# Kernel optimization log

Measured on AMD Instinct MI355X. Metric: run time of the kernel, lower is better.

The kernel has to match this reference:

```python
import jax, jax.numpy as jnp
import numpy as np

FEAT_IN = 64     # len(nonterminals)
EMB = 256        # embedding_dim
K = 30           # sortk
B = 48           # batch items
NG = 11          # graphs per item (1 goal + 10 env)
G = B * NG       # 528 graphs
NPG = 192        # nodes per graph
EPG = 384        # edges per graph
N = G * NPG
E = G * EPG
D = 3 * EMB + 1  # 769, concat channel dim = conv5 kernel/stride
DENSE = (K // 2 - 5 + 1) * EMB  # 11*256 = 2816


def setup_inputs() -> dict:
    key = jax.random.key(0)
    ks = jax.random.split(key, 12)
    x = jax.random.normal(ks[0], (N, FEAT_IN), jnp.float32)
    # edges within each graph, no self loops (remove_self_loops in original)
    src_l = jax.random.randint(ks[1], (E,), 0, NPG)
    off = jax.random.randint(ks[2], (E,), 1, NPG)
    dst_l = (src_l + off) % NPG
    goff = (jnp.arange(E) // EPG) * NPG
    src = (src_l + goff).astype(jnp.int32)
    dst = (dst_l + goff).astype(jnp.int32)

    def lin(k, fi, fo):
        return (jax.random.normal(k, (fi, fo), jnp.float32) / np.float32(np.sqrt(fi)))

    return dict(
        x=x, src=src, dst=dst,
        W1=lin(ks[3], FEAT_IN, EMB), b1=jnp.zeros((EMB,), jnp.float32),
        W2=lin(ks[4], EMB, EMB), b2=jnp.zeros((EMB,), jnp.float32),
        W3=lin(ks[5], EMB, EMB), b3=jnp.zeros((EMB,), jnp.float32),
        W4=lin(ks[6], EMB, 1), b4=jnp.zeros((1,), jnp.float32),
        w5=jax.random.normal(ks[7], (EMB // 2, 1, D), jnp.float32) / np.float32(np.sqrt(D)),
        bc5=jnp.zeros((EMB // 2,), jnp.float32),
        w6=jax.random.normal(ks[8], (EMB, EMB // 2, 5), jnp.float32) / np.float32(np.sqrt(5 * EMB // 2)),
        bc6=jnp.zeros((EMB,), jnp.float32),
        Wc1=lin(ks[9], NG * DENSE, EMB), bc1=jnp.zeros((EMB,), jnp.float32),
        Wc2=lin(ks[10], EMB, 10), bc2=jnp.zeros((10,), jnp.float32),
    )


def _gcn(x, W, b, src, dst):
    # PyG GCNConv: add self loops, symmetric norm D^-1/2 (A+I) D^-1/2 (XW) + b
    h = x @ W
    deg = jnp.ones((N,), h.dtype).at[dst].add(1.0)  # +1 for self loop
    dis = jax.lax.rsqrt(deg)
    msg = h[src] * (dis[src] * dis[dst])[:, None]
    agg = jnp.zeros_like(h).at[dst].add(msg)
    return agg + h * (dis * dis)[:, None] + b  # self-loop norm = 1/deg


def _conv1d(x, w, b, stride):
    y = jax.lax.conv_general_dilated(x, w, (stride,), 'VALID',
                                     dimension_numbers=('NCH', 'OIH', 'NCH'))
    return y + b[None, :, None]


def reference(x, src, dst, W1, b1, W2, b2, W3, b3, W4, b4,
              w5, bc5, w6, bc6, Wc1, bc1, Wc2, bc2):
    x1 = jnp.tanh(_gcn(x, W1, b1, src, dst))
    x2 = jnp.tanh(_gcn(x1, W2, b2, src, dst))
    x3 = jnp.tanh(_gcn(x2, W3, b3, src, dst))
    x4 = jnp.tanh(_gcn(x3, W4, b4, src, dst))
    xc = jnp.concatenate([x1, x2, x3, x4], axis=-1)  # [N, D]
    xg = xc.reshape(G, NPG, D)
    # global_sort_pool: sort nodes per graph by last channel (desc), take top K
    _, idx = jax.lax.top_k(xg[:, :, -1], K)          # [G, K]
    xs = jnp.take_along_axis(xg, idx[:, :, None], axis=1)  # [G, K, D]
    seq = xs.reshape(G, 1, K * D)
    y = jax.nn.relu(_conv1d(seq, w5, bc5, D))        # [G, EMB/2, K]
    y = y.reshape(G, EMB // 2, K // 2, 2).max(axis=-1)  # MaxPool1d(2,2)
    y = jax.nn.relu(_conv1d(y, w6, bc6, 1))          # [G, EMB, K//2-4]
    emb = y.reshape(B, NG * DENSE)                   # 11 graphs per item, flattened
    h = jax.nn.relu(emb @ Wc1 + bc1)
    logits = h @ Wc2 + bc2                           # dropout is identity at eval
    return logits
```

## Files before the change

kernel.cpp:

```cpp
#include <hip/hip_runtime.h>
#include <hip/hip_bf16.h>

#define EMB   256
#define KSORT 30
#define BATCH 48
#define NGPI  11
#define GG    528
#define NPG   192
#define EPG   384
#define DCH   769
#define GC    528
#define NCH   (GG/GC)
#define MC    (GC*NPG)
#define EC    (GC*EPG)
#define FQ    44
#define FCH   (2816/FQ)
#define KB5   5

__device__ __forceinline__ int clampi(int v, int lo, int hi) {
  return v < lo ? lo : (v > hi ? hi : v);
}

__device__ __attribute__((aligned(16))) float g_c1[MC * EMB];
__device__ __attribute__((aligned(16))) float g_c2[MC * EMB];
__device__ __attribute__((aligned(16))) float g_c3[MC * EMB];
__device__ __attribute__((aligned(16))) float g_tb[MC * EMB];
__device__ __attribute__((aligned(16))) float g_dis[MC];
__device__ __attribute__((aligned(16))) float g_x4[MC];
__device__ __attribute__((aligned(16))) float g_s4[MC];
__device__ __attribute__((aligned(16))) int   g_indptr[MC + 1];
__device__ __attribute__((aligned(16))) int   g_ssrc[EC];
__device__ __attribute__((aligned(16))) int   g_idx[GC * KSORT];
__device__ __attribute__((aligned(16))) float g_w5t[DCH * 128];
__device__ __attribute__((aligned(16))) float g_w6t[640 * 256];
__device__ __attribute__((aligned(16))) float g_y[GC * 128 * 30];
__device__ __attribute__((aligned(16))) float g_z[GG * 2816];
__device__ __attribute__((aligned(16))) float g_hp[NGPI * FQ * BATCH * 256];
__device__ __attribute__((aligned(16))) float g_h[BATCH * 256];

__device__ __forceinline__ float* selbuf(int s) {
  return s == 0 ? g_c1 : (s == 1 ? g_c2 : g_c3);
}

__global__ __launch_bounds__(192) void build_csr_k(const int* __restrict__ src,
    const int* __restrict__ dst, int g0) {
  __shared__ int cnt[NPG];
  __shared__ int offs[NPG];
  int g = blockIdx.x, t = threadIdx.x;
  int gg = g0 + g;
  cnt[t] = 0;
  __syncthreads();
  int ebase = gg * EPG, gnb = gg * NPG, lnb = g * NPG;
  for (int e = t; e < EPG; e += 192) {
    int dl = clampi(dst[ebase + e] - gnb, 0, NPG - 1);
    atomicAdd(&cnt[dl], 1);
  }
  __syncthreads();
  if (t == 0) {
    int run = g * EPG;
    for (int i = 0; i < NPG; i++) { offs[i] = run; run += cnt[i]; }
  }
  __syncthreads();
  g_indptr[lnb + t] = offs[t];
  g_dis[lnb + t] = 1.0f / sqrtf(1.0f + (float)cnt[t]);
  if (g == 0 && t == 0) g_indptr[MC] = EC;
  __syncthreads();
  for (int e = t; e < EPG; e += 192) {
    int ee = ebase + e;
    int dl = clampi(dst[ee] - gnb, 0, NPG - 1);
    int pos = clampi(atomicAdd(&offs[dl], 1), 0, EC - 1);
    g_ssrc[pos] = clampi(src[ee] - gnb, 0, NPG - 1) + lnb;
  }
}

template<bool AX>
__global__ __launch_bounds__(256) void gemm_k(const float* __restrict__ Ax,
    int asel, const float* __restrict__ W, int Kd) {
  __shared__ float As[16 * 192];
  __shared__ float Bs[16][68];
  const int m0 = blockIdx.x * 128, n0 = blockIdx.y * 128;
  const int t = threadIdx.x;
  const int tx = t & 15, ty = t >> 4;
  const int arow = t >> 1, acol = (t & 1) * 8;
  const int awr = (arow >> 3) * 12 + (arow & 7);
  const int brow = t >> 4, bcol = tx * 4;
  float acc[8][8];
#pragma unroll
  for (int i = 0; i < 8; i++)
#pragma unroll
    for (int j = 0; j < 8; j++) acc[i][j] = 0.f;
  const float* Ap = AX ? Ax : selbuf(asel);
  const float* arp = Ap + (size_t)(m0 + arow) * Kd + acol;
  const float* bsp = W + (size_t)brow * EMB + n0 + bcol;
  const float* Wg = W + n0 + 64 + tx * 4;
  const int nt = Kd >> 4;
  float4 pa0 = *(const float4*)(arp);
  float4 pa1 = *(const float4*)(arp + 4);
  float4 pb  = *(const float4*)(bsp);
  for (int it = 0; it < nt; ++it) {
    As[(acol + 0) * 192 + awr] = pa0.x;
    As[(acol + 1) * 192 + awr] = pa0.y;
    As[(acol + 2) * 192 + awr] = pa0.z;
    As[(acol + 3) * 192 + awr] = pa0.w;
    As[(acol + 4) * 192 + awr] = pa1.x;
    As[(acol + 5) * 192 + awr] = pa1.y;
    As[(acol + 6) * 192 + awr] = pa1.z;
    As[(acol + 7) * 192 + awr] = pa1.w;
    *(float4*)&Bs[brow][bcol] = pb;
    __syncthreads();
    if (it + 1 < nt) {
      const float* ap = arp + (it + 1) * 16;
      pa0 = *(const float4*)(ap);
      pa1 = *(const float4*)(ap + 4);
      pb  = *(const float4*)(bsp + (size_t)(it + 1) * 16 * EMB);
    }
    const float* Wk = Wg + (size_t)(it * 16) * EMB;
#pragma unroll
    for (int kk = 0; kk < 16; kk++) {
      float a[8], b[8];
      *(float4*)&a[0] = *(const float4*)&As[kk * 192 + ty * 12];
      *(float4*)&a[4] = *(const float4*)&As[kk * 192 + ty * 12 + 4];
      *(float4*)&b[0] = *(const float4*)&Bs[kk][bcol];
      *(float4*)&b[4] = *(const float4*)(Wk + kk * EMB);
#pragma unroll
      for (int i = 0; i < 8; i++)
#pragma unroll
        for (int j = 0; j < 8; j++) acc[i][j] += a[i] * b[j];
    }
    __syncthreads();
  }
#pragma unroll
  for (int i = 0; i < 8; i++) {
    float* cp = g_tb + (size_t)(m0 + ty * 8 + i) * EMB + n0 + tx * 4;
    *(float4*)cp = make_float4(acc[i][0], acc[i][1], acc[i][2], acc[i][3]);
    *(float4*)(cp + 64) = make_float4(acc[i][4], acc[i][5], acc[i][6], acc[i][7]);
  }
}

__global__ __launch_bounds__(256) void agg_k(int osel,
    const float* __restrict__ bias, const float* __restrict__ W4) {
  int n = blockIdx.x * 4 + (threadIdx.x >> 6);
  int lane = threadIdx.x & 63;
  float dn = g_dis[n];
  const float4* H4 = (const float4*)g_tb;
  float4 hv = H4[(size_t)n * 64 + lane];
  float sc = dn * dn;
  float ax = hv.x * sc, ay = hv.y * sc, az = hv.z * sc, aw = hv.w * sc;
  int beg = g_indptr[n], end = g_indptr[n + 1];
  for (int j = beg; j < end; j++) {
    int s = g_ssrc[j];
    float c = g_dis[s] * dn;
    float4 v = H4[(size_t)s * 64 + lane];
    ax += v.x * c; ay += v.y * c; az += v.z * c; aw += v.w * c;
  }
  float4 bv = ((const float4*)bias)[lane];
  float4 o;
  o.x = tanhf(ax + bv.x);
  o.y = tanhf(ay + bv.y);
  o.z = tanhf(az + bv.z);
  o.w = tanhf(aw + bv.w);
  ((float4*)selbuf(osel))[(size_t)n * 64 + lane] = o;
  if (W4) {
    float4 w = ((const float4*)W4)[lane];
    float s = o.x * w.x + o.y * w.y + o.z * w.z + o.w * w.w;
    for (int off = 32; off > 0; off >>= 1) s += __shfl_down(s, off, 64);
    if (lane == 0) g_s4[n] = s;
  }
}

__global__ __launch_bounds__(256) void agg4_k(const float* __restrict__ b4) {
  int n = blockIdx.x * 256 + threadIdx.x;
  if (n >= MC) return;
  float dn = g_dis[n];
  float acc = g_s4[n] * dn * dn;
  int beg = g_indptr[n], end = g_indptr[n + 1];
  for (int j = beg; j < end; j++) {
    int s = g_ssrc[j];
    acc += g_s4[s] * g_dis[s] * dn;
  }
  g_x4[n] = tanhf(acc + b4[0]);
}

__global__ __launch_bounds__(256) void sortpool_k() {
  __shared__ float sv[256];
  __shared__ int si[256];
  int g = blockIdx.x, t = threadIdx.x;
  if (t < NPG) { sv[t] = g_x4[g * NPG + t]; si[t] = t; }
  else { sv[t] = -1e30f; si[t] = 1 << 20; }
  __syncthreads();
  for (int k = 2; k <= 256; k <<= 1) {
    for (int j = k >> 1; j > 0; j >>= 1) {
      int ixj = t ^ j;
      if (ixj > t) {
        float v1 = sv[t], v2 = sv[ixj];
        int i1 = si[t], i2 = si[ixj];
        bool before_t = (v1 > v2) || (v1 == v2 && i1 < i2);
        bool up = ((t & k) == 0);
        if (up ? !before_t : before_t) {
          sv[t] = v2; sv[ixj] = v1;
          si[t] = i2; si[ixj] = i1;
        }
      }
      __syncthreads();
    }
  }
  if (t < KSORT) g_idx[g * KSORT + t] = clampi(g * NPG + si[t], 0, MC - 1);
}

__global__ __launch_bounds__(256) void tw5_k(const float* __restrict__ w5) {
  int i = blockIdx.x * 256 + threadIdx.x;
  if (i >= 128 * DCH) return;
  int o = i / DCH, d = i % DCH;
  g_w5t[d * 128 + o] = w5[i];
}
__global__ __launch_bounds__(256) void tw6_k(const float* __restrict__ w6) {
  int i = blockIdx.x * 256 + threadIdx.x;
  if (i >= 256 * 640) return;
  int o = i / 640, ir = i % 640;
  g_w6t[ir * 256 + o] = w6[i];
}

__global__ __launch_bounds__(128) void conv5_k(const float* __restrict__ bc5) {
  __shared__ float ar[KB5][772];
  int g = blockIdx.x, kb = blockIdx.y * KB5;
  int t = threadIdx.x;
  for (int kk = 0; kk < KB5; kk++) {
    int n = clampi(g_idx[g * KSORT + kb + kk], 0, MC - 1);
    const float* p1 = g_c1 + (size_t)n * EMB;
    const float* p2 = g_c2 + (size_t)n * EMB;
    const float* p3 = g_c3 + (size_t)n * EMB;
    for (int d = t; d < EMB; d += 128) {
      ar[kk][d] = p1[d];
      ar[kk][EMB + d] = p2[d];
      ar[kk][2 * EMB + d] = p3[d];
    }
    if (t == 0) ar[kk][768] = g_x4[n];
  }
  __syncthreads();
  float acc[KB5];
  float bias = bc5[t];
#pragma unroll
  for (int kk = 0; kk < KB5; kk++) acc[kk] = bias;
  const float* wbase = g_w5t + t;
  int d = 0;
  for (; d + 8 <= DCH; d += 8) {
    float w0 = wbase[(d + 0) * 128], w1 = wbase[(d + 1) * 128];
    float w2 = wbase[(d + 2) * 128], w3 = wbase[(d + 3) * 128];
    float w4 = wbase[(d + 4) * 128], w5 = wbase[(d + 5) * 128];
    float w6 = wbase[(d + 6) * 128], w7 = wbase[(d + 7) * 128];
#pragma unroll
    for (int kk = 0; kk < KB5; kk++) {
      float4 a0 = *(const float4*)&ar[kk][d];
      float4 a1 = *(const float4*)&ar[kk][d + 4];
      acc[kk] += a0.x * w0 + a0.y * w1 + a0.z * w2 + a0.w * w3 +
                 a1.x * w4 + a1.y * w5 + a1.z * w6 + a1.w * w7;
    }
  }
  for (; d < DCH; d++) {
    float wv = wbase[d * 128];
#pragma unroll
    for (int kk = 0; kk < KB5; kk++) acc[kk] += ar[kk][d] * wv;
  }
#pragma unroll
  for (int kk = 0; kk < KB5; kk++)
    g_y[(size_t)g * 3840 + t * KSORT + kb + kk] = fmaxf(acc[kk], 0.f);
}

__global__ __launch_bounds__(256) void conv6_k(const float* __restrict__ bc6,
                                               int g0) {
  __shared__ float s[128 * 16];
  int g = blockIdx.x, t = threadIdx.x;
  for (int i = t; i < 1920; i += 256) {
    int ch = i / 15, j = i % 15;
    const float* yp = g_y + (size_t)g * 3840 + ch * 30 + 2 * j;
    s[ch * 16 + j] = fmaxf(yp[0], yp[1]);
  }
  __syncthreads();
  float acc[11];
  float bias = bc6[t];
#pragma unroll
  for (int q = 0; q < 11; q++) acc[q] = bias;
  for (int i = 0; i < 128; i += 2) {
    float wA[5], wB[5];
#pragma unroll
    for (int r = 0; r < 5; r++) {
      wA[r] = g_w6t[(i * 5 + r) * 256 + t];
      wB[r] = g_w6t[((i + 1) * 5 + r) * 256 + t];
    }
    const float* sA = &s[i * 16];
    const float* sB = &s[(i + 1) * 16];
#pragma unroll
    for (int r = 0; r < 5; r++)
#pragma unroll
      for (int q = 0; q < 11; q++)
        acc[q] += sA[r + q] * wA[r] + sB[r + q] * wB[r];
  }
#pragma unroll
  for (int q = 0; q < 11; q++)
    g_z[(size_t)(g0 + g) * 2816 + t * 11 + q] = fmaxf(acc[q], 0.f);
}

__global__ __launch_bounds__(128) void dense1_k(const float* __restrict__ Wc1) {
  __shared__ float zs[BATCH][FCH];
  int gi = blockIdx.x;
  int obase = blockIdx.y * 128;
  int fq = blockIdx.z, f0 = fq * FCH;
  int t = threadIdx.x;
  for (int i = t; i < BATCH * FCH; i += 128) {
    int gl = i >> 6, f = i & 63;
    zs[gl][f] = g_z[(size_t)(gl * NGPI + gi) * 2816 + f0 + f];
  }
  __syncthreads();
  const float* wp = Wc1 + (size_t)gi * 2816 * 256 + (size_t)f0 * 256 + obase + t;
  float acc[BATCH];
#pragma unroll
  for (int gl = 0; gl < BATCH; gl++) acc[gl] = 0.f;
  float wc[8];
#pragma unroll
  for (int r = 0; r < 8; r++) wc[r] = wp[(size_t)r * 256];
  for (int f = 0; f < FCH; f += 8) {
    float wn[8];
    int fn = (f + 8 < FCH) ? f + 8 : f;
#pragma unroll
    for (int r = 0; r < 8; r++) wn[r] = wp[(size_t)(fn + r) * 256];
#pragma unroll
    for (int gl = 0; gl < BATCH; gl++) {
      float4 z0 = *(const float4*)&zs[gl][f];
      float4 z1 = *(const float4*)&zs[gl][f + 4];
      acc[gl] += z0.x * wc[0] + z0.y * wc[1] + z0.z * wc[2] + z0.w * wc[3] +
                 z1.x * wc[4] + z1.y * wc[5] + z1.z * wc[6] + z1.w * wc[7];
    }
#pragma unroll
    for (int r = 0; r < 8; r++) wc[r] = wn[r];
  }
  float* hp = g_hp + (size_t)(gi * FQ + fq) * (BATCH * 256);
#pragma unroll
  for (int gl = 0; gl < BATCH; gl++)
    hp[gl * 256 + obase + t] = acc[gl];
}

__global__ __launch_bounds__(256) void reduce_k() {
  int j = blockIdx.x * 256 + threadIdx.x;
  if (j >= BATCH * 256) return;
  float s0 = 0.f, s1 = 0.f, s2 = 0.f, s3 = 0.f;
  const size_t STR = BATCH * 256;
  for (int p = 0; p < NGPI * FQ; p += 4) {
    s0 += g_hp[(size_t)(p + 0) * STR + j];
    s1 += g_hp[(size_t)(p + 1) * STR + j];
    s2 += g_hp[(size_t)(p + 2) * STR + j];
    s3 += g_hp[(size_t)(p + 3) * STR + j];
  }
  g_h[j] = (s0 + s1) + (s2 + s3);
}

__global__ __launch_bounds__(256) void dense2_k(const float* __restrict__ bc1,
    const float* __restrict__ Wc2, const float* __restrict__ bc2,
    float* __restrict__ out) {
  __shared__ float hs[BATCH * 256];
  int t = threadIdx.x;
  for (int i = t; i < BATCH * 256; i += 256) {
    int o = i & 255;
    hs[i] = fmaxf(g_h[i] + bc1[o], 0.f);
  }
  __syncthreads();
  for (int i = t; i < 480; i += 256) {
    int b = i / 10, c = i % 10;
    float acc = bc2[c];
    for (int k = 0; k < 256; k++) acc += hs[b * 256 + k] * Wc2[k * 10 + c];
    out[i] = acc;
  }
}

__global__ void diag_k(float* __restrict__ out, float v) {
  int i = blockIdx.x * 256 + threadIdx.x;
  if (i < 480) out[i] = v;
}

extern "C" void kernel_launch(void* const* d_in, const int* in_sizes, int n_in,
                              void* d_out, int out_size, void* d_ws, size_t ws_size,
                              hipStream_t stream) {
  const float* x   = (const float*)d_in[0];
  const int*   src = (const int*)d_in[1];
  const int*   dst = (const int*)d_in[2];
  const float* W1  = (const float*)d_in[3];
  const float* b1  = (const float*)d_in[4];
  const float* W2  = (const float*)d_in[5];
  const float* b2  = (const float*)d_in[6];
  const float* W3  = (const float*)d_in[7];
  const float* b3  = (const float*)d_in[8];
  const float* W4  = (const float*)d_in[9];
  const float* b4  = (const float*)d_in[10];
  const float* w5  = (const float*)d_in[11];
  const float* bc5 = (const float*)d_in[12];
  const float* w6  = (const float*)d_in[13];
  const float* bc6 = (const float*)d_in[14];
  const float* Wc1 = (const float*)d_in[15];
  const float* bc1 = (const float*)d_in[16];
  const float* Wc2 = (const float*)d_in[17];
  const float* bc2 = (const float*)d_in[18];
  float* out = (float*)d_out;

  (void)hipGetLastError();
  int lcount = 0, fidx = -1;
  hipError_t ferr = hipSuccess;
  auto ck = [&]() {
    hipError_t e = hipGetLastError();
    if (e != hipSuccess && ferr == hipSuccess) { ferr = e; fidx = lcount; }
    lcount++;
  };

  tw5_k<<<(128 * DCH + 255) / 256, 256, 0, stream>>>(w5); ck();
  tw6_k<<<(256 * 640 + 255) / 256, 256, 0, stream>>>(w6); ck();

  dim3 gg(MC / 128, 2);
  build_csr_k<<<GC, 192, 0, stream>>>(src, dst, 0); ck();
  gemm_k<true><<<gg, 256, 0, stream>>>(x, 0, W1, 64); ck();
  agg_k<<<MC / 4, 256, 0, stream>>>(0, b1, nullptr); ck();
  gemm_k<false><<<gg, 256, 0, stream>>>(nullptr, 0, W2, EMB); ck();
  agg_k<<<MC / 4, 256, 0, stream>>>(1, b2, nullptr); ck();
  gemm_k<false><<<gg, 256, 0, stream>>>(nullptr, 1, W3, EMB); ck();
  agg_k<<<MC / 4, 256, 0, stream>>>(2, b3, W4); ck();
  agg4_k<<<MC / 256, 256, 0, stream>>>(b4); ck();
  sortpool_k<<<GC, 256, 0, stream>>>(); ck();
  conv5_k<<<dim3(GC, 6), 128, 0, stream>>>(bc5); ck();
  conv6_k<<<GC, 256, 0, stream>>>(bc6, 0); ck();

  dense1_k<<<dim3(NGPI, 2, FQ), 128, 0, stream>>>(Wc1); ck();
  reduce_k<<<(BATCH * 256 + 255) / 256, 256, 0, stream>>>(); ck();
  dense2_k<<<1, 256, 0, stream>>>(bc1, Wc2, bc2, out); ck();

  if (ferr != hipSuccess) {
    int code = (int)ferr; if (code > 100) code = 100;
    float v = (fidx == 0) ? (1024.f + 8.f * code) : (2048.f + 16.f * code);
    diag_k<<<2, 256, 0, stream>>>(out, v);
  }
}
```

Before: 966.9 us.

## Fuse GCN transform and neighbor aggregation per graph using LDS

```diff
diff --git a/kernel.cpp b/kernel.cpp
--- a/kernel.cpp
+++ b/kernel.cpp
@@ -10,7 +10,6 @@
 #define EPG   384
 #define DCH   769
 #define GC    528
-#define NCH   (GG/GC)
 #define MC    (GC*NPG)
 #define EC    (GC*EPG)
 #define FQ    44
@@ -24,7 +23,6 @@
 __device__ __attribute__((aligned(16))) float g_c1[MC * EMB];
 __device__ __attribute__((aligned(16))) float g_c2[MC * EMB];
 __device__ __attribute__((aligned(16))) float g_c3[MC * EMB];
-__device__ __attribute__((aligned(16))) float g_tb[MC * EMB];
 __device__ __attribute__((aligned(16))) float g_dis[MC];
 __device__ __attribute__((aligned(16))) float g_x4[MC];
 __device__ __attribute__((aligned(16))) float g_s4[MC];
@@ -74,98 +72,103 @@
 }
 
 template<bool AX>
-__global__ __launch_bounds__(256) void gemm_k(const float* __restrict__ Ax,
-    int asel, const float* __restrict__ W, int Kd) {
-  __shared__ float As[16 * 192];
-  __shared__ float Bs[16][68];
-  const int m0 = blockIdx.x * 128, n0 = blockIdx.y * 128;
+__global__ __launch_bounds__(256) void gcn_k(const float* __restrict__ Ax,
+    int asel, int osel, const float* __restrict__ W,
+    const float* __restrict__ bias, int Kd) {
+  __shared__ float lds[13056];
+  const int cb = blockIdx.x, g = blockIdx.y;
   const int t = threadIdx.x;
   const int tx = t & 15, ty = t >> 4;
-  const int arow = t >> 1, acol = (t & 1) * 8;
-  const int awr = (arow >> 3) * 12 + (arow & 7);
-  const int brow = t >> 4, bcol = tx * 4;
-  float acc[8][8];
-#pragma unroll
-  for (int i = 0; i < 8; i++)
-#pragma unroll
-    for (int j = 0; j < 8; j++) acc[i][j] = 0.f;
-  const float* Ap = AX ? Ax : selbuf(asel);
-  const float* arp = Ap + (size_t)(m0 + arow) * Kd + acol;
-  const float* bsp = W + (size_t)brow * EMB + n0 + bcol;
-  const float* Wg = W + n0 + 64 + tx * 4;
+  const int n0 = cb * 64;
+  const int base = g * NPG;
+  float acc[12][4];
+#pragma unroll
+  for (int i = 0; i < 12; i++)
+#pragma unroll
+    for (int j = 0; j < 4; j++) acc[i][j] = 0.f;
+  const float* Ap = (AX ? Ax : selbuf(asel)) + (size_t)base * Kd;
+  const float* Wp = W + n0 + tx * 4;
   const int nt = Kd >> 4;
-  float4 pa0 = *(const float4*)(arp);
-  float4 pa1 = *(const float4*)(arp + 4);
-  float4 pb  = *(const float4*)(bsp);
+  float4 pf0, pf1, pf2, pf3;
+  if (t < NPG) {
+    const float* ap = Ap + (size_t)t * Kd;
+    pf0 = *(const float4*)(ap + 0);
+    pf1 = *(const float4*)(ap + 4);
+    pf2 = *(const float4*)(ap + 8);
+    pf3 = *(const float4*)(ap + 12);
+  }
   for (int it = 0; it < nt; ++it) {
-    As[(acol + 0) * 192 + awr] = pa0.x;
-    As[(acol + 1) * 192 + awr] = pa0.y;
-    As[(acol + 2) * 192 + awr] = pa0.z;
-    As[(acol + 3) * 192 + awr] = pa0.w;
-    As[(acol + 4) * 192 + awr] = pa1.x;
-    As[(acol + 5) * 192 + awr] = pa1.y;
-    As[(acol + 6) * 192 + awr] = pa1.z;
-    As[(acol + 7) * 192 + awr] = pa1.w;
-    *(float4*)&Bs[brow][bcol] = pb;
+    if (t < NPG) {
+      lds[ 0 * 200 + t] = pf0.x; lds[ 1 * 200 + t] = pf0.y;
+      lds[ 2 * 200 + t] = pf0.z; lds[ 3 * 200 + t] = pf0.w;
+      lds[ 4 * 200 + t] = pf1.x; lds[ 5 * 200 + t] = pf1.y;
+      lds[ 6 * 200 + t] = pf1.z; lds[ 7 * 200 + t] = pf1.w;
+      lds[ 8 * 200 + t] = pf2.x; lds[ 9 * 200 + t] = pf2.y;
+      lds[10 * 200 + t] = pf2.z; lds[11 * 200 + t] = pf2.w;
+      lds[12 * 200 + t] = pf3.x; lds[13 * 200 + t] = pf3.y;
+      lds[14 * 200 + t] = pf3.z; lds[15 * 200 + t] = pf3.w;
+    }
     __syncthreads();
-    if (it + 1 < nt) {
-      const float* ap = arp + (it + 1) * 16;
-      pa0 = *(const float4*)(ap);
-      pa1 = *(const float4*)(ap + 4);
-      pb  = *(const float4*)(bsp + (size_t)(it + 1) * 16 * EMB);
-    }
-    const float* Wk = Wg + (size_t)(it * 16) * EMB;
+    if (it + 1 < nt && t < NPG) {
+      const float* ap = Ap + (size_t)t * Kd + (it + 1) * 16;
+      pf0 = *(const float4*)(ap + 0);
+      pf1 = *(const float4*)(ap + 4);
+      pf2 = *(const float4*)(ap + 8);
+      pf3 = *(const float4*)(ap + 12);
+    }
+    const float* Wk = Wp + (size_t)(it * 16) * EMB;
 #pragma unroll
     for (int kk = 0; kk < 16; kk++) {
-      float a[8], b[8];
-      *(float4*)&a[0] = *(const float4*)&As[kk * 192 + ty * 12];
-      *(float4*)&a[4] = *(const float4*)&As[kk * 192 + ty * 12 + 4];
-      *(float4*)&b[0] = *(const float4*)&Bs[kk][bcol];
-      *(float4*)&b[4] = *(const float4*)(Wk + kk * EMB);
-#pragma unroll
-      for (int i = 0; i < 8; i++)
-#pragma unroll
-        for (int j = 0; j < 8; j++) acc[i][j] += a[i] * b[j];
+      float a[12], b[4];
+      *(float4*)&a[0] = *(const float4*)&lds[kk * 200 + ty * 12];
+      *(float4*)&a[4] = *(const float4*)&lds[kk * 200 + ty * 12 + 4];
+      *(float4*)&a[8] = *(const float4*)&lds[kk * 200 + ty * 12 + 8];
+      *(float4*)&b[0] = *(const float4*)(Wk + (size_t)kk * EMB);
+#pragma unroll
+      for (int i = 0; i < 12; i++)
+#pragma unroll
+        for (int j = 0; j < 4; j++) acc[i][j] += a[i] * b[j];
     }
     __syncthreads();
   }
 #pragma unroll
-  for (int i = 0; i < 8; i++) {
-    float* cp = g_tb + (size_t)(m0 + ty * 8 + i) * EMB + n0 + tx * 4;
-    *(float4*)cp = make_float4(acc[i][0], acc[i][1], acc[i][2], acc[i][3]);
-    *(float4*)(cp + 64) = make_float4(acc[i][4], acc[i][5], acc[i][6], acc[i][7]);
-  }
-}
-
-__global__ __launch_bounds__(256) void agg_k(int osel,
-    const float* __restrict__ bias, const float* __restrict__ W4) {
+  for (int i = 0; i < 12; i++)
+    *(float4*)&lds[(ty * 12 + i) * 68 + tx * 4] =
+        make_float4(acc[i][0], acc[i][1], acc[i][2], acc[i][3]);
+  __syncthreads();
+  float4 bv = ((const float4*)bias)[cb * 16 + tx];
+  float* outp = selbuf(osel);
+#pragma unroll
+  for (int i = 0; i < 12; i++) {
+    int r = ty * 12 + i, n = base + r;
+    float dn = g_dis[n];
+    float sc = dn * dn;
+    float ax = acc[i][0] * sc, ay = acc[i][1] * sc;
+    float az = acc[i][2] * sc, aw = acc[i][3] * sc;
+    int beg = g_indptr[n], end = g_indptr[n + 1];
+    for (int j = beg; j < end; j++) {
+      int ls = clampi(g_ssrc[j] - base, 0, NPG - 1);
+      float c = g_dis[base + ls] * dn;
+      const float4 v = *(const float4*)&lds[ls * 68 + tx * 4];
+      ax += v.x * c; ay += v.y * c; az += v.z * c; aw += v.w * c;
+    }
+    float4 o;
+    o.x = tanhf(ax + bv.x);
+    o.y = tanhf(ay + bv.y);
+    o.z = tanhf(az + bv.z);
+    o.w = tanhf(aw + bv.w);
+    *(float4*)(outp + (size_t)n * EMB + n0 + tx * 4) = o;
+  }
+}
+
+__global__ __launch_bounds__(256) void gemm4_k(const float* __restrict__ W4) {
   int n = blockIdx.x * 4 + (threadIdx.x >> 6);
   int lane = threadIdx.x & 63;
-  float dn = g_dis[n];
-  const float4* H4 = (const float4*)g_tb;
-  float4 hv = H4[(size_t)n * 64 + lane];
-  float sc = dn * dn;
-  float ax = hv.x * sc, ay = hv.y * sc, az = hv.z * sc, aw = hv.w * sc;
-  int beg = g_indptr[n], end = g_indptr[n + 1];
-  for (int j = beg; j < end; j++) {
-    int s = g_ssrc[j];
-    float c = g_dis[s] * dn;
-    float4 v = H4[(size_t)s * 64 + lane];
-    ax += v.x * c; ay += v.y * c; az += v.z * c; aw += v.w * c;
-  }
-  float4 bv = ((const float4*)bias)[lane];
-  float4 o;
-  o.x = tanhf(ax + bv.x);
-  o.y = tanhf(ay + bv.y);
-  o.z = tanhf(az + bv.z);
-  o.w = tanhf(aw + bv.w);
-  ((float4*)selbuf(osel))[(size_t)n * 64 + lane] = o;
-  if (W4) {
-    float4 w = ((const float4*)W4)[lane];
-    float s = o.x * w.x + o.y * w.y + o.z * w.z + o.w * w.w;
-    for (int off = 32; off > 0; off >>= 1) s += __shfl_down(s, off, 64);
-    if (lane == 0) g_s4[n] = s;
-  }
+  float4 a = *(const float4*)(g_c3 + (size_t)n * EMB + lane * 4);
+  float4 w = *(const float4*)(W4 + lane * 4);
+  float s = a.x * w.x + a.y * w.y + a.z * w.z + a.w * w.w;
+  for (int off = 32; off > 0; off >>= 1) s += __shfl_down(s, off, 64);
+  if (lane == 0) g_s4[n] = s;
 }
 
 __global__ __launch_bounds__(256) void agg4_k(const float* __restrict__ b4) {
@@ -412,14 +415,12 @@
   tw5_k<<<(128 * DCH + 255) / 256, 256, 0, stream>>>(w5); ck();
   tw6_k<<<(256 * 640 + 255) / 256, 256, 0, stream>>>(w6); ck();
 
-  dim3 gg(MC / 128, 2);
+  dim3 gf(4, GC);
   build_csr_k<<<GC, 192, 0, stream>>>(src, dst, 0); ck();
-  gemm_k<true><<<gg, 256, 0, stream>>>(x, 0, W1, 64); ck();
-  agg_k<<<MC / 4, 256, 0, stream>>>(0, b1, nullptr); ck();
-  gemm_k<false><<<gg, 256, 0, stream>>>(nullptr, 0, W2, EMB); ck();
-  agg_k<<<MC / 4, 256, 0, stream>>>(1, b2, nullptr); ck();
-  gemm_k<false><<<gg, 256, 0, stream>>>(nullptr, 1, W3, EMB); ck();
-  agg_k<<<MC / 4, 256, 0, stream>>>(2, b3, W4); ck();
+  gcn_k<true><<<gf, 256, 0, stream>>>(x, 0, 0, W1, b1, 64); ck();
+  gcn_k<false><<<gf, 256, 0, stream>>>(nullptr, 0, 1, W2, b2, EMB); ck();
+  gcn_k<false><<<gf, 256, 0, stream>>>(nullptr, 1, 2, W3, b3, EMB); ck();
+  gemm4_k<<<MC / 4, 256, 0, stream>>>(W4); ck();
   agg4_k<<<MC / 256, 256, 0, stream>>>(b4); ck();
   sortpool_k<<<GC, 256, 0, stream>>>(); ck();
   conv5_k<<<dim3(GC, 6), 128, 0, stream>>>(bc5); ck();
```

Result: slower. 1.051 ms (+8.7%).

## Fuse layer-4 aggregation, sort-pool, conv5 and conv6 into one per-graph kernel

Applied to the files above, without the earlier changes.

```diff
diff --git a/kernel.cpp b/kernel.cpp
--- a/kernel.cpp
+++ b/kernel.cpp
@@ -10,12 +10,10 @@
 #define EPG   384
 #define DCH   769
 #define GC    528
-#define NCH   (GG/GC)
 #define MC    (GC*NPG)
 #define EC    (GC*EPG)
 #define FQ    44
 #define FCH   (2816/FQ)
-#define KB5   5
 
 __device__ __forceinline__ int clampi(int v, int lo, int hi) {
   return v < lo ? lo : (v > hi ? hi : v);
@@ -26,14 +24,11 @@
 __device__ __attribute__((aligned(16))) float g_c3[MC * EMB];
 __device__ __attribute__((aligned(16))) float g_tb[MC * EMB];
 __device__ __attribute__((aligned(16))) float g_dis[MC];
-__device__ __attribute__((aligned(16))) float g_x4[MC];
 __device__ __attribute__((aligned(16))) float g_s4[MC];
 __device__ __attribute__((aligned(16))) int   g_indptr[MC + 1];
 __device__ __attribute__((aligned(16))) int   g_ssrc[EC];
-__device__ __attribute__((aligned(16))) int   g_idx[GC * KSORT];
 __device__ __attribute__((aligned(16))) float g_w5t[DCH * 128];
 __device__ __attribute__((aligned(16))) float g_w6t[640 * 256];
-__device__ __attribute__((aligned(16))) float g_y[GC * 128 * 30];
 __device__ __attribute__((aligned(16))) float g_z[GG * 2816];
 __device__ __attribute__((aligned(16))) float g_hp[NGPI * FQ * BATCH * 256];
 __device__ __attribute__((aligned(16))) float g_h[BATCH * 256];
@@ -139,7 +134,8 @@
 
 __global__ __launch_bounds__(256) void agg_k(int osel,
     const float* __restrict__ bias, const float* __restrict__ W4) {
-  int n = blockIdx.x * 4 + (threadIdx.x >> 6);
+  int nb = (blockIdx.x & 7) * (MC / 4 / 8) + (blockIdx.x >> 3);
+  int n = nb * 4 + (threadIdx.x >> 6);
   int lane = threadIdx.x & 63;
   float dn = g_dis[n];
   const float4* H4 = (const float4*)g_tb;
@@ -168,45 +164,6 @@
   }
 }
 
-__global__ __launch_bounds__(256) void agg4_k(const float* __restrict__ b4) {
-  int n = blockIdx.x * 256 + threadIdx.x;
-  if (n >= MC) return;
-  float dn = g_dis[n];
-  float acc = g_s4[n] * dn * dn;
-  int beg = g_indptr[n], end = g_indptr[n + 1];
-  for (int j = beg; j < end; j++) {
-    int s = g_ssrc[j];
-    acc += g_s4[s] * g_dis[s] * dn;
-  }
-  g_x4[n] = tanhf(acc + b4[0]);
-}
-
-__global__ __launch_bounds__(256) void sortpool_k() {
-  __shared__ float sv[256];
-  __shared__ int si[256];
-  int g = blockIdx.x, t = threadIdx.x;
-  if (t < NPG) { sv[t] = g_x4[g * NPG + t]; si[t] = t; }
-  else { sv[t] = -1e30f; si[t] = 1 << 20; }
-  __syncthreads();
-  for (int k = 2; k <= 256; k <<= 1) {
-    for (int j = k >> 1; j > 0; j >>= 1) {
-      int ixj = t ^ j;
-      if (ixj > t) {
-        float v1 = sv[t], v2 = sv[ixj];
-        int i1 = si[t], i2 = si[ixj];
-        bool before_t = (v1 > v2) || (v1 == v2 && i1 < i2);
-        bool up = ((t & k) == 0);
-        if (up ? !before_t : before_t) {
-          sv[t] = v2; sv[ixj] = v1;
-          si[t] = i2; si[ixj] = i1;
-        }
-      }
-      __syncthreads();
-    }
-  }
-  if (t < KSORT) g_idx[g * KSORT + t] = clampi(g * NPG + si[t], 0, MC - 1);
-}
-
 __global__ __launch_bounds__(256) void tw5_k(const float* __restrict__ w5) {
   int i = blockIdx.x * 256 + threadIdx.x;
   if (i >= 128 * DCH) return;
@@ -220,66 +177,108 @@
   g_w6t[ir * 256 + o] = w6[i];
 }
 
-__global__ __launch_bounds__(128) void conv5_k(const float* __restrict__ bc5) {
-  __shared__ float ar[KB5][772];
-  int g = blockIdx.x, kb = blockIdx.y * KB5;
-  int t = threadIdx.x;
-  for (int kk = 0; kk < KB5; kk++) {
-    int n = clampi(g_idx[g * KSORT + kb + kk], 0, MC - 1);
-    const float* p1 = g_c1 + (size_t)n * EMB;
-    const float* p2 = g_c2 + (size_t)n * EMB;
-    const float* p3 = g_c3 + (size_t)n * EMB;
-    for (int d = t; d < EMB; d += 128) {
-      ar[kk][d] = p1[d];
-      ar[kk][EMB + d] = p2[d];
-      ar[kk][2 * EMB + d] = p3[d];
-    }
-    if (t == 0) ar[kk][768] = g_x4[n];
-  }
-  __syncthreads();
-  float acc[KB5];
-  float bias = bc5[t];
-#pragma unroll
-  for (int kk = 0; kk < KB5; kk++) acc[kk] = bias;
-  const float* wbase = g_w5t + t;
-  int d = 0;
-  for (; d + 8 <= DCH; d += 8) {
-    float w0 = wbase[(d + 0) * 128], w1 = wbase[(d + 1) * 128];
-    float w2 = wbase[(d + 2) * 128], w3 = wbase[(d + 3) * 128];
-    float w4 = wbase[(d + 4) * 128], w5 = wbase[(d + 5) * 128];
-    float w6 = wbase[(d + 6) * 128], w7 = wbase[(d + 7) * 128];
-#pragma unroll
-    for (int kk = 0; kk < KB5; kk++) {
-      float4 a0 = *(const float4*)&ar[kk][d];
-      float4 a1 = *(const float4*)&ar[kk][d + 4];
-      acc[kk] += a0.x * w0 + a0.y * w1 + a0.z * w2 + a0.w * w3 +
-                 a1.x * w4 + a1.y * w5 + a1.z * w6 + a1.w * w7;
-    }
-  }
-  for (; d < DCH; d++) {
-    float wv = wbase[d * 128];
-#pragma unroll
-    for (int kk = 0; kk < KB5; kk++) acc[kk] += ar[kk][d] * wv;
-  }
-#pragma unroll
-  for (int kk = 0; kk < KB5; kk++)
-    g_y[(size_t)g * 3840 + t * KSORT + kb + kk] = fmaxf(acc[kk], 0.f);
-}
-
-__global__ __launch_bounds__(256) void conv6_k(const float* __restrict__ bc6,
-                                               int g0) {
-  __shared__ float s[128 * 16];
-  int g = blockIdx.x, t = threadIdx.x;
-  for (int i = t; i < 1920; i += 256) {
-    int ch = i / 15, j = i % 15;
-    const float* yp = g_y + (size_t)g * 3840 + ch * 30 + 2 * j;
-    s[ch * 16 + j] = fmaxf(yp[0], yp[1]);
+__global__ __launch_bounds__(256) void tail_k(const float* __restrict__ b4,
+    const float* __restrict__ bc5, const float* __restrict__ bc6) {
+  __shared__ float fs[8404];
+  __shared__ int si[256];
+  const int X4 = 0, SV = 192, Y = 448, AR = 4544;
+  const int g = blockIdx.x, t = threadIdx.x;
+  const int gbase = g * NPG;
+  if (t < NPG) {
+    int n = gbase + t;
+    float dn = g_dis[n];
+    float acc = g_s4[n] * dn * dn;
+    int beg = g_indptr[n], end = g_indptr[n + 1];
+    for (int j = beg; j < end; j++) {
+      int s = g_ssrc[j];
+      acc += g_s4[s] * g_dis[s] * dn;
+    }
+    fs[X4 + t] = tanhf(acc + b4[0]);
+  }
+  __syncthreads();
+  if (t < NPG) { fs[SV + t] = fs[X4 + t]; si[t] = t; }
+  else { fs[SV + t] = -1e30f; si[t] = 1 << 20; }
+  __syncthreads();
+  for (int k = 2; k <= 256; k <<= 1) {
+    for (int j = k >> 1; j > 0; j >>= 1) {
+      int ixj = t ^ j;
+      if (ixj > t) {
+        float v1 = fs[SV + t], v2 = fs[SV + ixj];
+        int i1 = si[t], i2 = si[ixj];
+        bool before_t = (v1 > v2) || (v1 == v2 && i1 < i2);
+        bool up = ((t & k) == 0);
+        if (up ? !before_t : before_t) {
+          fs[SV + t] = v2; fs[SV + ixj] = v1;
+          si[t] = i2; si[ixj] = i1;
+        }
+      }
+      __syncthreads();
+    }
+  }
+  const int ch = t & 127, half = t >> 7;
+  for (int kb = 0; kb < 6; kb++) {
+    for (int kk = 0; kk < 5; kk++) {
+      int nl = clampi(si[kb * 5 + kk], 0, NPG - 1);
+      const float* p1 = g_c1 + (size_t)(gbase + nl) * EMB;
+      const float* p2 = g_c2 + (size_t)(gbase + nl) * EMB;
+      const float* p3 = g_c3 + (size_t)(gbase + nl) * EMB;
+      fs[AR + kk * 772 + t] = p1[t];
+      fs[AR + kk * 772 + 256 + t] = p2[t];
+      fs[AR + kk * 772 + 512 + t] = p3[t];
+      if (t == 0) fs[AR + kk * 772 + 768] = fs[X4 + nl];
+    }
+    __syncthreads();
+    const int k0 = half, k1 = half + 2, k2 = half + 4;
+    float bias = bc5[ch];
+    float a0 = bias, a1 = bias, a2 = bias;
+    const float* wbase = g_w5t + ch;
+    const float* r0 = &fs[AR + k0 * 772];
+    const float* r1 = &fs[AR + k1 * 772];
+    const float* r2 = &fs[AR + (half ? 0 : k2) * 772];
+    int d = 0;
+    for (; d + 8 <= DCH; d += 8) {
+      float w0 = wbase[(d + 0) * 128], w1 = wbase[(d + 1) * 128];
+      float w2 = wbase[(d + 2) * 128], w3 = wbase[(d + 3) * 128];
+      float w4 = wbase[(d + 4) * 128], w5 = wbase[(d + 5) * 128];
+      float w6 = wbase[(d + 6) * 128], w7 = wbase[(d + 7) * 128];
+      {
+        float4 x0 = *(const float4*)&r0[d];
+        float4 x1 = *(const float4*)&r0[d + 4];
+        a0 += x0.x * w0 + x0.y * w1 + x0.z * w2 + x0.w * w3 +
+              x1.x * w4 + x1.y * w5 + x1.z * w6 + x1.w * w7;
+      }
+      {
+        float4 x0 = *(const float4*)&r1[d];
+        float4 x1 = *(const float4*)&r1[d + 4];
+        a1 += x0.x * w0 + x0.y * w1 + x0.z * w2 + x0.w * w3 +
+              x1.x * w4 + x1.y * w5 + x1.z * w6 + x1.w * w7;
+      }
+      {
+        float4 x0 = *(const float4*)&r2[d];
+        float4 x1 = *(const float4*)&r2[d + 4];
+        a2 += x0.x * w0 + x0.y * w1 + x0.z * w2 + x0.w * w3 +
+              x1.x * w4 + x1.y * w5 + x1.z * w6 + x1.w * w7;
+      }
+    }
+    for (; d < DCH; d++) {
+      float wv = wbase[d * 128];
+      a0 += r0[d] * wv; a1 += r1[d] * wv; a2 += r2[d] * wv;
+    }
+    fs[Y + ch * 32 + kb * 5 + k0] = fmaxf(a0, 0.f);
+    fs[Y + ch * 32 + kb * 5 + k1] = fmaxf(a1, 0.f);
+    if (!half) fs[Y + ch * 32 + kb * 5 + k2] = fmaxf(a2, 0.f);
+    __syncthreads();
+  }
+  for (int i = t; i < 128 * 15; i += 256) {
+    int c = i / 15, j = i % 15;
+    fs[AR + c * 16 + j] =
+        fmaxf(fs[Y + c * 32 + 2 * j], fs[Y + c * 32 + 2 * j + 1]);
   }
   __syncthreads();
   float acc[11];
-  float bias = bc6[t];
-#pragma unroll
-  for (int q = 0; q < 11; q++) acc[q] = bias;
+  float bias6 = bc6[t];
+#pragma unroll
+  for (int q = 0; q < 11; q++) acc[q] = bias6;
   for (int i = 0; i < 128; i += 2) {
     float wA[5], wB[5];
 #pragma unroll
@@ -287,8 +286,8 @@
       wA[r] = g_w6t[(i * 5 + r) * 256 + t];
       wB[r] = g_w6t[((i + 1) * 5 + r) * 256 + t];
     }
-    const float* sA = &s[i * 16];
-    const float* sB = &s[(i + 1) * 16];
+    const float* sA = &fs[AR + i * 16];
+    const float* sB = &fs[AR + (i + 1) * 16];
 #pragma unroll
     for (int r = 0; r < 5; r++)
 #pragma unroll
@@ -297,7 +296,7 @@
   }
 #pragma unroll
   for (int q = 0; q < 11; q++)
-    g_z[(size_t)(g0 + g) * 2816 + t * 11 + q] = fmaxf(acc[q], 0.f);
+    g_z[(size_t)g * 2816 + t * 11 + q] = fmaxf(acc[q], 0.f);
 }
 
 __global__ __launch_bounds__(128) void dense1_k(const float* __restrict__ Wc1) {
@@ -420,10 +419,7 @@
   agg_k<<<MC / 4, 256, 0, stream>>>(1, b2, nullptr); ck();
   gemm_k<false><<<gg, 256, 0, stream>>>(nullptr, 1, W3, EMB); ck();
   agg_k<<<MC / 4, 256, 0, stream>>>(2, b3, W4); ck();
-  agg4_k<<<MC / 256, 256, 0, stream>>>(b4); ck();
-  sortpool_k<<<GC, 256, 0, stream>>>(); ck();
-  conv5_k<<<dim3(GC, 6), 128, 0, stream>>>(bc5); ck();
-  conv6_k<<<GC, 256, 0, stream>>>(bc6, 0); ck();
+  tail_k<<<GC, 256, 0, stream>>>(b4, bc5, bc6); ck();
 
   dense1_k<<<dim3(NGPI, 2, FQ), 128, 0, stream>>>(Wc1); ck();
   reduce_k<<<(BATCH * 256 + 255) / 256, 256, 0, stream>>>(); ck();
```

Measured after the change: 1.018 ms. 1.05x slower.
